# Optimization experiments

Hardware: AMD Instinct MI355X
Metric: run time of the kernel (lower is better)

## Reference

```python
import jax, jax.numpy as jnp
import numpy as np

NUM_EXPERTS = 16
IN_FEATURES = 2048
OUT_FEATURES = 2048
RANK = 128
ALPHA = 32.0
TOKENS = 32768  # total packed tokens, multiple of NUM_EXPERTS (pad_seq_to_mult guarantees this)


def setup_inputs() -> dict:
    key = jax.random.key(0)
    k1, k2, k3 = jax.random.split(key, 3)
    x = jax.random.normal(k1, (TOKENS, IN_FEATURES), dtype=jnp.float32)
    # linear_in per-expert weights (kaiming-style random for reference)
    lora_a = jax.random.normal(k2, (NUM_EXPERTS, IN_FEATURES, RANK), dtype=jnp.float32) * (1.0 / np.sqrt(IN_FEATURES))
    # linear_out per-expert weights (LoRA convention init is zeros; random here for nontrivial check)
    lora_b = jax.random.normal(k3, (NUM_EXPERTS, RANK, OUT_FEATURES), dtype=jnp.float32) * (1.0 / np.sqrt(RANK))
    return {"x": x, "lora_a": lora_a, "lora_b": lora_b}


def reference(x, lora_a, lora_b):
    # Tokens are packed per expert with uniform counts (padding to a multiple of
    # NUM_EXPERTS is handled upstream by pad_seq_to_mult). Grouped LoRA:
    #   out_e = (x_e @ A_e) @ B_e * (alpha / rank)
    E = lora_a.shape[0]
    T, H = x.shape
    xg = x.reshape(E, T // E, H)                      # [E, Te, H]
    low = jnp.einsum('eth,ehr->etr', xg, lora_a)      # grouped GEMM 1: [E, Te, r]
    # activation = identity (adapter default)
    out = jnp.einsum('etr,ero->eto', low, lora_b)     # grouped GEMM 2: [E, Te, O]
    scale = ALPHA / RANK
    return (out * scale).reshape(T, -1)               # [T, O]
```

## Files before the change

kernel.cpp:

```cpp
#include <hip/hip_runtime.h>
#include <hip/hip_bf16.h>
#include <stdint.h>

#define NEXP   16
#define TTOK   32768
#define HIN    2048
#define RNK    128
#define OOUT   2048
#define BM     64
#define LORA_SCALE 0.25f

typedef __bf16 bf16_t;
typedef bf16_t bf16x8 __attribute__((ext_vector_type(8)));
typedef bf16_t bf16x4 __attribute__((ext_vector_type(4)));
typedef float  f32x4  __attribute__((ext_vector_type(4)));

__global__ void transpose_cvt_kernel(const float* __restrict__ src,
                                     bf16_t* __restrict__ dst,
                                     int Rr, int Cc)
{
    __shared__ float tile[32][33];
    const int e  = blockIdx.z;
    const int c0 = blockIdx.x * 32;
    const int r0 = blockIdx.y * 32;
    const float* s = src + (size_t)e * Rr * Cc;
    bf16_t*      d = dst + (size_t)e * Rr * Cc;
    const int tx = threadIdx.x & 31;
    const int ty = threadIdx.x >> 5;
#pragma unroll
    for (int j = 0; j < 32; j += 8)
        tile[ty + j][tx] = s[(size_t)(r0 + ty + j) * Cc + (c0 + tx)];
    __syncthreads();
#pragma unroll
    for (int j = 0; j < 32; j += 8)
        d[(size_t)(c0 + ty + j) * Rr + (r0 + tx)] = (bf16_t)tile[tx][ty + j];
}

__global__ __launch_bounds__(512, 4)
void fused_lora(const float* __restrict__ X,
                const bf16_t* __restrict__ Atw,
                const bf16_t* __restrict__ Btw,
                float* __restrict__ Out)
{
    __shared__ __align__(16) char lds[65536];

    const int tid = threadIdx.x;
    const int bid = blockIdx.x;
    const int blk = (bid & 7) * 64 + (bid >> 3);
    const int m0  = blk * BM;
    const int e   = blk >> 5;

    const int wave = tid >> 6;
    const int lane = tid & 63;
    const int lm   = lane & 15;
    const int q    = lane >> 4;
    const int wr   = (wave & 1) * 32;
    const int wc   = (wave >> 1) * 32;

    const int sxr = tid >> 3, sxc = tid & 7;
    const int sar = tid >> 2, sac = tid & 3;

    const float*  xg = X   + (size_t)(m0 + sxr) * HIN + sxc * 8;
    const bf16_t* ag = Atw + ((size_t)e * RNK + sar) * HIN + sac * 16;

    f32x4  xa0, xa1;
    bf16x8 ar0, ar1;
    f32x4  acc1[2][2] = {};

    {
        xa0 = *(const f32x4*)(xg);
        xa1 = *(const f32x4*)(xg + 4);
        ar0 = *(const bf16x8*)(ag);
        ar1 = *(const bf16x8*)(ag + 8);
        bf16x8 cx;
#pragma unroll
        for (int i = 0; i < 4; ++i) { cx[i] = (bf16_t)xa0[i]; cx[4 + i] = (bf16_t)xa1[i]; }
        const int xsw = (sxr & 7) << 4, asw = (sar & 7) << 4;
        *(bf16x8*)(lds + sxr * 128 + ((sxc * 16) ^ xsw)) = cx;
        *(bf16x8*)(lds + 16384 + sar * 128 + ((sac * 32     ) ^ asw)) = ar0;
        *(bf16x8*)(lds + 16384 + sar * 128 + ((sac * 32 + 16) ^ asw)) = ar1;
    }
    __syncthreads();

    for (int it = 0; it < 32; ++it) {
        const int cur = it & 1;
        if (it < 31) {
            const float*  px = xg + (it + 1) * 64;
            const bf16_t* pa = ag + (it + 1) * 64;
            xa0 = *(const f32x4*)px;
            xa1 = *(const f32x4*)(px + 4);
            ar0 = *(const bf16x8*)pa;
            ar1 = *(const bf16x8*)(pa + 8);
        }
        const char* xb = lds + cur * 8192;
        const char* ab = lds + 16384 + cur * 16384;
#pragma unroll
        for (int ks = 0; ks < 2; ++ks) {
            bf16x8 XF[2], AF[2];
#pragma unroll
            for (int mt = 0; mt < 2; ++mt) {
                const int row = wr + mt * 16 + lm;
                XF[mt] = *(const bf16x8*)(xb + row * 128 +
                           ((ks * 64 + q * 16) ^ ((row & 7) << 4)));
            }
#pragma unroll
            for (int ct = 0; ct < 2; ++ct) {
                const int row = wc + ct * 16 + lm;
                AF[ct] = *(const bf16x8*)(ab + row * 128 +
                           ((ks * 64 + q * 16) ^ ((row & 7) << 4)));
            }
#pragma unroll
            for (int mt = 0; mt < 2; ++mt)
#pragma unroll
                for (int ct = 0; ct < 2; ++ct)
                    acc1[mt][ct] = __builtin_amdgcn_mfma_f32_16x16x32_bf16(
                        AF[ct], XF[mt], acc1[mt][ct], 0, 0, 0);
        }
        if (it < 31) {
            bf16x8 cx;
#pragma unroll
            for (int i = 0; i < 4; ++i) { cx[i] = (bf16_t)xa0[i]; cx[4 + i] = (bf16_t)xa1[i]; }
            const int xsw = (sxr & 7) << 4, asw = (sar & 7) << 4;
            *(bf16x8*)(lds + (cur ^ 1) * 8192 + sxr * 128 + ((sxc * 16) ^ xsw)) = cx;
            *(bf16x8*)(lds + 16384 + (cur ^ 1) * 16384 + sar * 128 + ((sac * 32     ) ^ asw)) = ar0;
            *(bf16x8*)(lds + 16384 + (cur ^ 1) * 16384 + sar * 128 + ((sac * 32 + 16) ^ asw)) = ar1;
        }
        __syncthreads();
    }

    bf16x8 br[4];
    const bf16_t* bg0 = Btw + ((size_t)e * OOUT + sar) * RNK + sac * 32;
#pragma unroll
    for (int i = 0; i < 4; ++i) br[i] = *(const bf16x8*)(bg0 + i * 8);

    char* Lb = lds + 49152;
#pragma unroll
    for (int mt = 0; mt < 2; ++mt) {
        const int m   = wr + mt * 16 + lm;
        const int msw = (m & 7) << 4;
#pragma unroll
        for (int ct = 0; ct < 2; ++ct) {
            const int r0 = wc + ct * 16 + q * 4;
            bf16x4 v;
#pragma unroll
            for (int i = 0; i < 4; ++i) v[i] = (bf16_t)acc1[mt][ct][i];
            *(bf16x4*)(Lb + m * 256 + ((r0 * 2) ^ msw)) = v;
        }
    }
    __syncthreads();

    bf16x8 af2[2][4];
#pragma unroll
    for (int mt = 0; mt < 2; ++mt) {
        const int m   = wr + mt * 16 + lm;
        const int msw = (m & 7) << 4;
#pragma unroll
        for (int ks = 0; ks < 4; ++ks)
            af2[mt][ks] = *(const bf16x8*)(Lb + m * 256 + ((ks * 64 + q * 16) ^ msw));
    }

    {
        char* bb = lds + sar * 256;
        const int bsw = (sar & 7) << 4;
#pragma unroll
        for (int i = 0; i < 4; ++i)
            *(bf16x8*)(bb + ((sac * 64 + i * 16) ^ bsw)) = br[i];
    }
    __syncthreads();

    for (int c = 0; c < 16; ++c) {
        const int cur = c & 1;
        if (c < 15) {
            const bf16_t* bg = bg0 + (size_t)(c + 1) * 128 * RNK;
#pragma unroll
            for (int i = 0; i < 4; ++i) br[i] = *(const bf16x8*)(bg + i * 8);
        }
        f32x4 acc2[2][2] = {};
        const char* bb = lds + cur * 32768;
#pragma unroll
        for (int nt = 0; nt < 2; ++nt) {
            const int n   = wc + nt * 16 + lm;
            const int nsw = (n & 7) << 4;
#pragma unroll
            for (int ks = 0; ks < 4; ++ks) {
                const bf16x8 BF = *(const bf16x8*)(bb + n * 256 +
                                     ((ks * 64 + q * 16) ^ nsw));
                acc2[0][nt] = __builtin_amdgcn_mfma_f32_16x16x32_bf16(
                    BF, af2[0][ks], acc2[0][nt], 0, 0, 0);
                acc2[1][nt] = __builtin_amdgcn_mfma_f32_16x16x32_bf16(
                    BF, af2[1][ks], acc2[1][nt], 0, 0, 0);
            }
        }
#pragma unroll
        for (int mt = 0; mt < 2; ++mt) {
            const int gm = m0 + wr + mt * 16 + lm;
            float* orow = Out + (size_t)gm * OOUT + c * 128 + wc + q * 4;
#pragma unroll
            for (int nt = 0; nt < 2; ++nt) {
                const f32x4 v = acc2[mt][nt] * LORA_SCALE;
                *(f32x4*)(orow + nt * 16) = v;
            }
        }
        if (c < 15) {
            char* bb2 = lds + (cur ^ 1) * 32768 + sar * 256;
            const int bsw = (sar & 7) << 4;
#pragma unroll
            for (int i = 0; i < 4; ++i)
                *(bf16x8*)(bb2 + ((sac * 64 + i * 16) ^ bsw)) = br[i];
        }
        __syncthreads();
    }
}

extern "C" void kernel_launch(void* const* d_in, const int* in_sizes, int n_in,
                              void* d_out, int out_size, void* d_ws, size_t ws_size,
                              hipStream_t stream)
{
    const float* x  = (const float*)d_in[0];
    const float* la = (const float*)d_in[1];
    const float* lb = (const float*)d_in[2];
    float* out = (float*)d_out;

    bf16_t* At  = (bf16_t*)d_ws;
    bf16_t* Btw = At + (size_t)NEXP * RNK * HIN;

    {
        dim3 g(RNK / 32, HIN / 32, NEXP);
        transpose_cvt_kernel<<<g, 256, 0, stream>>>(la, At, HIN, RNK);
    }
    {
        dim3 g(OOUT / 32, RNK / 32, NEXP);
        transpose_cvt_kernel<<<g, 256, 0, stream>>>(lb, Btw, RNK, OOUT);
    }
    fused_lora<<<dim3(TTOK / BM), dim3(512), 0, stream>>>(x, At, Btw, out);
}
```

Baseline: 503.8 us.

## Deepen global prefetch to two stages and use LDS-only barriers

Both GEMM phases now prefetch global tiles two iterations ahead using two alternating register sets, instead of one iteration ahead. The manual unroll by two keeps the register sets static. `__syncthreads` is replaced by a barrier that waits only on LDS counters (`lgkmcnt(0)`), so outstanding global loads can stay in flight across iterations. This targets global-load latency stalls in a latency-bound loop, at the cost of more registers, which may lower occupancy.

```diff
diff --git a/kernel.cpp b/kernel.cpp
--- a/kernel.cpp
+++ b/kernel.cpp
@@ -14,6 +14,8 @@
 typedef bf16_t bf16x8 __attribute__((ext_vector_type(8)));
 typedef bf16_t bf16x4 __attribute__((ext_vector_type(4)));
 typedef float  f32x4  __attribute__((ext_vector_type(4)));
+
+#define BARRIER() asm volatile("s_waitcnt lgkmcnt(0)\n\ts_barrier" ::: "memory")
 
 __global__ void transpose_cvt_kernel(const float* __restrict__ src,
                                      bf16_t* __restrict__ dst,
@@ -59,41 +61,47 @@
 
     const int sxr = tid >> 3, sxc = tid & 7;
     const int sar = tid >> 2, sac = tid & 3;
+    const int xsw = (sxr & 7) << 4;
+    const int asw = (sar & 7) << 4;
 
     const float*  xg = X   + (size_t)(m0 + sxr) * HIN + sxc * 8;
     const bf16_t* ag = Atw + ((size_t)e * RNK + sar) * HIN + sac * 16;
 
-    f32x4  xa0, xa1;
-    bf16x8 ar0, ar1;
+    char* XsBase = lds;
+    char* AsBase = lds + 16384;
+    char* Lb     = lds + 49152;
+
+    f32x4  xA0, xA1, xB0, xB1;
+    bf16x8 aA0, aA1, aB0, aB1;
     f32x4  acc1[2][2] = {};
 
-    {
-        xa0 = *(const f32x4*)(xg);
-        xa1 = *(const f32x4*)(xg + 4);
-        ar0 = *(const bf16x8*)(ag);
-        ar1 = *(const bf16x8*)(ag + 8);
+    xA0 = *(const f32x4*)(xg);        xA1 = *(const f32x4*)(xg + 4);
+    aA0 = *(const bf16x8*)(ag);       aA1 = *(const bf16x8*)(ag + 8);
+    xB0 = *(const f32x4*)(xg + 64);   xB1 = *(const f32x4*)(xg + 68);
+    aB0 = *(const bf16x8*)(ag + 64);  aB1 = *(const bf16x8*)(ag + 72);
+    {
         bf16x8 cx;
 #pragma unroll
-        for (int i = 0; i < 4; ++i) { cx[i] = (bf16_t)xa0[i]; cx[4 + i] = (bf16_t)xa1[i]; }
-        const int xsw = (sxr & 7) << 4, asw = (sar & 7) << 4;
-        *(bf16x8*)(lds + sxr * 128 + ((sxc * 16) ^ xsw)) = cx;
-        *(bf16x8*)(lds + 16384 + sar * 128 + ((sac * 32     ) ^ asw)) = ar0;
-        *(bf16x8*)(lds + 16384 + sar * 128 + ((sac * 32 + 16) ^ asw)) = ar1;
-    }
-    __syncthreads();
-
-    for (int it = 0; it < 32; ++it) {
+        for (int i = 0; i < 4; ++i) { cx[i] = (bf16_t)xA0[i]; cx[4 + i] = (bf16_t)xA1[i]; }
+        *(bf16x8*)(XsBase + sxr * 128 + ((sxc * 16) ^ xsw)) = cx;
+        *(bf16x8*)(AsBase + sar * 128 + ((sac * 32     ) ^ asw)) = aA0;
+        *(bf16x8*)(AsBase + sar * 128 + ((sac * 32 + 16) ^ asw)) = aA1;
+    }
+    BARRIER();
+
+    auto p1_step = [&](int it,
+                       f32x4& lx0, f32x4& lx1, bf16x8& la0, bf16x8& la1,
+                       f32x4& sx0, f32x4& sx1, bf16x8& sa0, bf16x8& sa1)
+    {
         const int cur = it & 1;
-        if (it < 31) {
-            const float*  px = xg + (it + 1) * 64;
-            const bf16_t* pa = ag + (it + 1) * 64;
-            xa0 = *(const f32x4*)px;
-            xa1 = *(const f32x4*)(px + 4);
-            ar0 = *(const bf16x8*)pa;
-            ar1 = *(const bf16x8*)(pa + 8);
-        }
-        const char* xb = lds + cur * 8192;
-        const char* ab = lds + 16384 + cur * 16384;
+        if (it < 30) {
+            const float*  px = xg + (size_t)(it + 2) * 64;
+            const bf16_t* pa = ag + (size_t)(it + 2) * 64;
+            lx0 = *(const f32x4*)px;   lx1 = *(const f32x4*)(px + 4);
+            la0 = *(const bf16x8*)pa;  la1 = *(const bf16x8*)(pa + 8);
+        }
+        const char* xb = XsBase + cur * 8192;
+        const char* ab = AsBase + cur * 16384;
 #pragma unroll
         for (int ks = 0; ks < 2; ++ks) {
             bf16x8 XF[2], AF[2];
@@ -119,21 +127,26 @@
         if (it < 31) {
             bf16x8 cx;
 #pragma unroll
-            for (int i = 0; i < 4; ++i) { cx[i] = (bf16_t)xa0[i]; cx[4 + i] = (bf16_t)xa1[i]; }
-            const int xsw = (sxr & 7) << 4, asw = (sar & 7) << 4;
-            *(bf16x8*)(lds + (cur ^ 1) * 8192 + sxr * 128 + ((sxc * 16) ^ xsw)) = cx;
-            *(bf16x8*)(lds + 16384 + (cur ^ 1) * 16384 + sar * 128 + ((sac * 32     ) ^ asw)) = ar0;
-            *(bf16x8*)(lds + 16384 + (cur ^ 1) * 16384 + sar * 128 + ((sac * 32 + 16) ^ asw)) = ar1;
-        }
-        __syncthreads();
-    }
-
-    bf16x8 br[4];
+            for (int i = 0; i < 4; ++i) { cx[i] = (bf16_t)sx0[i]; cx[4 + i] = (bf16_t)sx1[i]; }
+            *(bf16x8*)(XsBase + (cur ^ 1) * 8192 + sxr * 128 + ((sxc * 16) ^ xsw)) = cx;
+            *(bf16x8*)(AsBase + (cur ^ 1) * 16384 + sar * 128 + ((sac * 32     ) ^ asw)) = sa0;
+            *(bf16x8*)(AsBase + (cur ^ 1) * 16384 + sar * 128 + ((sac * 32 + 16) ^ asw)) = sa1;
+        }
+        BARRIER();
+    };
+
+    for (int it2 = 0; it2 < 16; ++it2) {
+        p1_step(2 * it2,     xA0, xA1, aA0, aA1,  xB0, xB1, aB0, aB1);
+        p1_step(2 * it2 + 1, xB0, xB1, aB0, aB1,  xA0, xA1, aA0, aA1);
+    }
+
+    bf16x8 bA[4], bB[4];
     const bf16_t* bg0 = Btw + ((size_t)e * OOUT + sar) * RNK + sac * 32;
 #pragma unroll
-    for (int i = 0; i < 4; ++i) br[i] = *(const bf16x8*)(bg0 + i * 8);
-
-    char* Lb = lds + 49152;
+    for (int i = 0; i < 4; ++i) bA[i] = *(const bf16x8*)(bg0 + i * 8);
+#pragma unroll
+    for (int i = 0; i < 4; ++i) bB[i] = *(const bf16x8*)(bg0 + (size_t)128 * RNK + i * 8);
+
 #pragma unroll
     for (int mt = 0; mt < 2; ++mt) {
         const int m   = wr + mt * 16 + lm;
@@ -147,7 +160,7 @@
             *(bf16x4*)(Lb + m * 256 + ((r0 * 2) ^ msw)) = v;
         }
     }
-    __syncthreads();
+    BARRIER();
 
     bf16x8 af2[2][4];
 #pragma unroll
@@ -161,19 +174,19 @@
 
     {
         char* bb = lds + sar * 256;
-        const int bsw = (sar & 7) << 4;
 #pragma unroll
         for (int i = 0; i < 4; ++i)
-            *(bf16x8*)(bb + ((sac * 64 + i * 16) ^ bsw)) = br[i];
-    }
-    __syncthreads();
-
-    for (int c = 0; c < 16; ++c) {
+            *(bf16x8*)(bb + ((sac * 64 + i * 16) ^ asw)) = bA[i];
+    }
+    BARRIER();
+
+    auto p2_step = [&](int c, bf16x8* lset, bf16x8* sset)
+    {
         const int cur = c & 1;
-        if (c < 15) {
-            const bf16_t* bg = bg0 + (size_t)(c + 1) * 128 * RNK;
-#pragma unroll
-            for (int i = 0; i < 4; ++i) br[i] = *(const bf16x8*)(bg + i * 8);
+        if (c < 14) {
+            const bf16_t* bg = bg0 + (size_t)(c + 2) * 128 * RNK;
+#pragma unroll
+            for (int i = 0; i < 4; ++i) lset[i] = *(const bf16x8*)(bg + i * 8);
         }
         f32x4 acc2[2][2] = {};
         const char* bb = lds + cur * 32768;
@@ -203,12 +216,16 @@
         }
         if (c < 15) {
             char* bb2 = lds + (cur ^ 1) * 32768 + sar * 256;
-            const int bsw = (sar & 7) << 4;
 #pragma unroll
             for (int i = 0; i < 4; ++i)
-                *(bf16x8*)(bb2 + ((sac * 64 + i * 16) ^ bsw)) = br[i];
-        }
-        __syncthreads();
+                *(bf16x8*)(bb2 + ((sac * 64 + i * 16) ^ asw)) = sset[i];
+        }
+        BARRIER();
+    };
+
+    for (int c2 = 0; c2 < 8; ++c2) {
+        p2_step(2 * c2,     bA, bB);
+        p2_step(2 * c2 + 1, bB, bA);
     }
 }
 
```

New measurement: 515.2 us. +2.3%, slower.
